# Optimization experiments

Measured on AMD Instinct MI355X. Metric: run time of the kernel, lower is better.

The kernel has to match this reference:

```python
import jax, jax.numpy as jnp
import numpy as np

E = 2048
H = 16
D = E // H  # head_dim = 128
S_SLOTS = 8
EPS = 1e-5


def _linear_params(key, fan_in, fan_out):
    kw, kb = jax.random.split(key)
    lim = 1.0 / np.sqrt(fan_in)
    W = jax.random.uniform(kw, (fan_out, fan_in), jnp.float32, -lim, lim)
    b = jax.random.uniform(kb, (fan_out,), jnp.float32, -lim, lim)
    return W, b


def setup_inputs() -> dict:
    key = jax.random.key(0)
    ks = jax.random.split(key, 10)
    x = jax.random.normal(ks[0], (2, 2048, E), jnp.float32)
    thought_slots = jax.random.normal(ks[1], (S_SLOTS, E), jnp.float32)
    Wq, bq = _linear_params(ks[2], E, E)
    Wk, bk = _linear_params(ks[3], E, E)
    Wv, bv = _linear_params(ks[4], E, E)
    Wtq, btq = _linear_params(ks[5], E, E)
    Wtk, btk = _linear_params(ks[6], E, E)
    Wtv, btv = _linear_params(ks[7], E, E)
    Wo, bo = _linear_params(ks[8], E, E)
    gamma = jnp.ones((E,), jnp.float32)
    beta = jnp.zeros((E,), jnp.float32)
    return dict(x=x, thought_slots=thought_slots, Wq=Wq, bq=bq, Wk=Wk, bk=bk,
                Wv=Wv, bv=bv, Wtq=Wtq, btq=btq, Wtk=Wtk, btk=btk,
                Wtv=Wtv, btv=btv, Wo=Wo, bo=bo, gamma=gamma, beta=beta)


def _heads(t, B):
    # [B, S, E] -> [B, H, S, D]
    return t.reshape(B, -1, H, D).transpose(0, 2, 1, 3)


def reference(x, thought_slots, Wq, bq, Wk, bk, Wv, bv,
              Wtq, btq, Wtk, btk, Wtv, btv, Wo, bo, gamma, beta):
    B, S, _ = x.shape
    scale = 1.0 / np.sqrt(D)

    # regular self-attention stream
    q = _heads(x @ Wq.T + bq, B)
    k = _heads(x @ Wk.T + bk, B)
    v = _heads(x @ Wv.T + bv, B)
    attn = jax.nn.softmax(jnp.einsum('bhqd,bhkd->bhqk', q, k) * scale, axis=-1)
    regular_out = jnp.einsum('bhqk,bhkd->bhqd', attn, v)

    # thought cross-attention stream (keys/values from learned slots)
    slots = jnp.broadcast_to(thought_slots, (B, S_SLOTS, thought_slots.shape[-1]))
    t_q = _heads(x @ Wtq.T + btq, B)
    t_k = _heads(slots @ Wtk.T + btk, B)
    t_v = _heads(slots @ Wtv.T + btv, B)
    t_attn = jax.nn.softmax(jnp.einsum('bhqd,bhkd->bhqk', t_q, t_k) * scale, axis=-1)
    thought_out = jnp.einsum('bhqk,bhkd->bhqd', t_attn, t_v)

    # merge heads, combine, layernorm, output projection
    combined = (regular_out + thought_out).transpose(0, 2, 1, 3).reshape(B, S, E)
    mu = jnp.mean(combined, axis=-1, keepdims=True)
    var = jnp.var(combined, axis=-1, keepdims=True)
    normed = (combined - mu) * jax.lax.rsqrt(var + EPS) * gamma + beta
    return normed @ Wo.T + bo
```

## Files before the change

### kernel.cpp

```cpp
#include <hip/hip_runtime.h>
#include <hip/hip_bf16.h>
#include <stdint.h>

typedef __bf16 bf16;
typedef __bf16 bf16x8 __attribute__((ext_vector_type(8)));
typedef __bf16 bf16x4 __attribute__((ext_vector_type(4)));
typedef float f32x4 __attribute__((ext_vector_type(4)));
typedef float f32x16 __attribute__((ext_vector_type(16)));
typedef uint32_t u32x2 __attribute__((ext_vector_type(2)));
typedef uint32_t u32x4 __attribute__((ext_vector_type(4)));

#define E_DIM 2048
#define HEADS 16
#define HD 128
#define SEQ 2048
#define BATCH 2
#define NTOK 4096
#define NSLOT 8

#define QSCALE (0.08838834764831845f * 1.4426950408889634f)

#define WAITV(N) asm volatile("s_waitcnt vmcnt(" #N ")" ::: "memory")

__device__ __forceinline__ void gload_lds16(const void* g, void* lds) {
  __builtin_amdgcn_global_load_lds(
      (const __attribute__((address_space(1))) uint32_t*)g,
      (__attribute__((address_space(3))) uint32_t*)lds, 16, 0, 0);
}

__global__ __launch_bounds__(256) void cvt_f32_bf16_kernel(
    const float* __restrict__ src, bf16* __restrict__ dst, int n8)
{
  for (int i = blockIdx.x * 256 + threadIdx.x; i < n8; i += gridDim.x * 256) {
    const f32x4 a = *(const f32x4*)(src + i * 8);
    const f32x4 b = *(const f32x4*)(src + i * 8 + 4);
    bf16x8 o;
#pragma unroll
    for (int j = 0; j < 4; j++) { o[j] = (bf16)a[j]; o[4 + j] = (bf16)b[j]; }
    *(bf16x8*)(dst + i * 8) = o;
  }
}

struct ProjArgs {
  const bf16* W[4];
  const float* bias[4];
  void* out[4];
  int mode[4];
  float scale[4];
};

__global__ __launch_bounds__(512, 2) void gemm256_kernel(
    const bf16* __restrict__ A, ProjArgs pa, int nbm, int nbn)
{
  __shared__ char As_[2 * 32768];
  __shared__ char Bs_[2 * 32768];

  const int nwg = gridDim.x;
  const int qch = nwg >> 3;
  const int wg = (blockIdx.x & 7) * qch + (blockIdx.x >> 3);
  const int bm = wg % nbm;
  const int rest = wg / nbm;
  const int bn = rest % nbn;
  const int z = rest / nbn;

  const bf16* __restrict__ W = pa.W[z];
  const float* __restrict__ bias = pa.bias[z];
  void* __restrict__ out = pa.out[z];
  const int mode = pa.mode[z];
  const float scale = pa.scale[z];

  const int tid = threadIdx.x;
  const int lane = tid & 63;
  const int w = tid >> 6;
  const int wr = w >> 2;
  const int wc = w & 3;
  const int g = lane >> 4, c = lane & 15;

  const int srow = tid >> 3;
  const int sslot = tid & 7;
  const int scol = (sslot ^ (srow & 7)) * 8;
  const bf16* Abase = A + (size_t)(bm * 256) * 2048;
  const bf16* Bbase = W + (size_t)(bn * 256) * 2048;

  auto stageU = [&](const bf16* gbase, char* lds, int T, int u) {
    char* dst = lds + (T & 1) * 32768 + u * 16384;
    const int k0 = T * 64;
#pragma unroll
    for (int j = 0; j < 2; j++) {
      const int r = u * 128 + srow + j * 64;
      gload_lds16(gbase + (size_t)r * 2048 + k0 + scol,
                  dst + (size_t)(srow + j * 64) * 128 + sslot * 16);
    }
  };

  f32x4 acc[8][4] = {};
  bf16x8 bfr[4][2];

  stageU(Bbase, Bs_, 0, 0); stageU(Bbase, Bs_, 0, 1);
  stageU(Abase, As_, 0, 0); stageU(Abase, As_, 0, 1);
  stageU(Bbase, Bs_, 1, 0); stageU(Bbase, Bs_, 1, 1);
  stageU(Abase, As_, 1, 0);
  WAITV(6);
  __builtin_amdgcn_s_barrier();

  const int NT = 2048 / 64;
  for (int t = 0; t < NT; t++) {
    const int d = t & 1;
    const char* Aq = As_ + d * 32768;
    const char* Bq = Bs_ + d * 32768;
#pragma unroll
    for (int q = 0; q < 4; q++) {
      bf16x8 af[2][2];
      if (q == 0) {
#pragma unroll
        for (int n = 0; n < 4; n++)
#pragma unroll
          for (int kk = 0; kk < 2; kk++) {
            const int row = wc * 64 + n * 16 + c;
            bfr[n][kk] = *(const bf16x8*)(Bq + (size_t)row * 128 +
                                          (((kk * 4 + g) ^ (c & 7)) * 16));
          }
      }
#pragma unroll
      for (int mi2 = 0; mi2 < 2; mi2++)
#pragma unroll
        for (int kk = 0; kk < 2; kk++) {
          const int row = wr * 128 + (q * 2 + mi2) * 16 + c;
          af[mi2][kk] = *(const bf16x8*)(Aq + (size_t)row * 128 +
                                         (((kk * 4 + g) ^ (c & 7)) * 16));
        }

      __builtin_amdgcn_s_barrier();

      if (q == 0)      { if (t + 1 < NT) stageU(Abase, As_, t + 1, 1); }
      else if (q == 1) { if (t + 2 < NT) stageU(Bbase, Bs_, t + 2, 0); }
      else if (q == 2) { if (t + 2 < NT) stageU(Bbase, Bs_, t + 2, 1); }
      else             { if (t + 2 < NT) stageU(Abase, As_, t + 2, 0); }

      __builtin_amdgcn_s_setprio(1);
#pragma unroll
      for (int mi2 = 0; mi2 < 2; mi2++)
#pragma unroll
        for (int n = 0; n < 4; n++)
#pragma unroll
          for (int kk = 0; kk < 2; kk++)
            acc[q * 2 + mi2][n] = __builtin_amdgcn_mfma_f32_16x16x32_bf16(
                af[mi2][kk], bfr[n][kk], acc[q * 2 + mi2][n], 0, 0, 0);
      __builtin_amdgcn_s_setprio(0);

      if (q == 3) {
        if (t < NT - 2)       { WAITV(6); }
        else if (t == NT - 2) { WAITV(0); }
      }
      __builtin_amdgcn_s_barrier();
    }
  }

#pragma unroll
  for (int mi = 0; mi < 8; mi++) {
#pragma unroll
    for (int n = 0; n < 4; n++) {
      const int col = bn * 256 + wc * 64 + n * 16 + c;
      const float bv = bias[col];
#pragma unroll
      for (int j = 0; j < 4; j++) {
        const int row = bm * 256 + wr * 128 + mi * 16 + g * 4 + j;
        const float v = (acc[mi][n][j] + bv) * scale;
        if (mode == 0) {
          ((float*)out)[(size_t)row * E_DIM + col] = v;
        } else {
          const int b = row >> 11, s = row & 2047;
          const int h = col >> 7, d2 = col & 127;
          size_t idx;
          if (mode == 1) idx = (((size_t)(b * HEADS + h)) * SEQ + s) * HD + d2;
          else           idx = (((size_t)(b * HEADS + h)) * HD + d2) * SEQ + s;
          ((bf16*)out)[idx] = (bf16)v;
        }
      }
    }
  }
}

__global__ __launch_bounds__(256) void gemm_nt_kernel(
    const bf16* __restrict__ A, ProjArgs pa, int M, int N, int K)
{
  __shared__ bf16 As[2][128 * 32];
  __shared__ bf16 Bs[2][128 * 32];

  const int z = blockIdx.z;
  const bf16* __restrict__ W = pa.W[z];
  const float* __restrict__ bias = pa.bias[z];
  void* __restrict__ out = pa.out[z];
  const int mode = pa.mode[z];
  const float scale = pa.scale[z];

  const int tid = threadIdx.x;
  const int lane = tid & 63;
  const int w = tid >> 6;
  const int wr = w >> 1, wc = w & 1;
  const int g = lane >> 4, c = lane & 15;
  const int bm = blockIdx.x, bn = blockIdx.y;

  f32x4 acc[4][4] = {};

  const int srow = lane >> 2;
  const int scol = (lane & 3) * 8;
  const bf16* Ab = A + (size_t)(bm * 128 + srow) * K + scol;
  const bf16* Wb = W + (size_t)(bn * 128 + srow) * K + scol;

  auto stage = [&](int k0, int buf) {
#pragma unroll
    for (int i = 0; i < 2; ++i) {
      const int chunk = w * 2 + i;
      gload_lds16(Ab + (size_t)(chunk * 16) * K + k0, (char*)(&As[buf][0]) + chunk * 1024);
      gload_lds16(Wb + (size_t)(chunk * 16) * K + k0, (char*)(&Bs[buf][0]) + chunk * 1024);
    }
  };

  stage(0, 0);
  __syncthreads();
  int cur = 0;

  for (int k0 = 0; k0 < K; k0 += 32) {
    if (k0 + 32 < K) stage(k0 + 32, cur ^ 1);
    bf16x8 af[4], bfr[4];
#pragma unroll
    for (int m = 0; m < 4; m++)
      af[m] = *(const bf16x8*)(&As[cur][0] + (wr * 64 + m * 16 + c) * 32 + g * 8);
#pragma unroll
    for (int n = 0; n < 4; n++)
      bfr[n] = *(const bf16x8*)(&Bs[cur][0] + (wc * 64 + n * 16 + c) * 32 + g * 8);
#pragma unroll
    for (int m = 0; m < 4; m++)
#pragma unroll
      for (int n = 0; n < 4; n++)
        acc[m][n] = __builtin_amdgcn_mfma_f32_16x16x32_bf16(af[m], bfr[n], acc[m][n], 0, 0, 0);
    __syncthreads();
    cur ^= 1;
  }

#pragma unroll
  for (int m = 0; m < 4; m++) {
#pragma unroll
    for (int n = 0; n < 4; n++) {
      const int col = bn * 128 + wc * 64 + n * 16 + c;
      const float bv = bias[col];
#pragma unroll
      for (int j = 0; j < 4; j++) {
        const int row = bm * 128 + wr * 64 + m * 16 + g * 4 + j;
        const float v = (acc[m][n][j] + bv) * scale;
        if (mode == 0) {
          ((float*)out)[(size_t)row * N + col] = v;
        } else {
          const int b = row >> 11, s = row & 2047;
          const int h = col >> 7, d = col & 127;
          size_t idx;
          if (mode == 1) idx = (((size_t)(b * HEADS + h)) * SEQ + s) * HD + d;
          else           idx = (((size_t)(b * HEADS + h)) * HD + d) * SEQ + s;
          ((bf16*)out)[idx] = (bf16)v;
        }
      }
    }
  }
}

__global__ __launch_bounds__(256) void slots_proj_kernel(
    const float* __restrict__ slots,
    const float* __restrict__ Wk, const float* __restrict__ bk,
    const float* __restrict__ Wv, const float* __restrict__ bv,
    float* __restrict__ tk, float* __restrict__ tv)
{
  const int col = blockIdx.x * 256 + threadIdx.x;
  const int slot = blockIdx.y;
  const int mat = blockIdx.z;
  const float* W = mat ? Wv : Wk;
  const float* bias = mat ? bv : bk;
  float* out = mat ? tv : tk;
  const float* xr = slots + (size_t)slot * E_DIM;
  const float* wr = W + (size_t)col * E_DIM;
  float acc = 0.f;
  for (int k = 0; k < E_DIM; k += 4) {
    const f32x4 a = *(const f32x4*)(xr + k);
    const f32x4 b4 = *(const f32x4*)(wr + k);
#pragma unroll
    for (int i = 0; i < 4; i++) acc += a[i] * b4[i];
  }
  out[(size_t)slot * E_DIM + col] = acc + bias[col];
}

__global__ __launch_bounds__(512) void flash_attn_kernel(
    const bf16* __restrict__ Qg, const bf16* __restrict__ Kg,
    const bf16* __restrict__ Vtg, bf16* __restrict__ Og)
{
  __shared__ char Ks[2][64 * 256];
  __shared__ char Vs[2][128 * 128];

  const int orig = blockIdx.x;
  const int logical = (orig & 7) * 32 + (orig >> 3);
  const int qt = logical & 7;
  const int bh = logical >> 3;

  const int tid = threadIdx.x;
  const int lane = tid & 63;
  const int w = tid >> 6;
  const int q = lane & 31;
  const int hi = lane >> 5;
  const int b = bh >> 4, h = bh & 15;
  const int q0 = qt * 256 + w * 32;

  const bf16* Qb = Qg + ((size_t)bh * SEQ + q0) * HD;
  const bf16* Kb = Kg + (size_t)bh * SEQ * HD;
  const bf16* Vb = Vtg + (size_t)bh * HD * SEQ;

  auto stage = [&](int kv0, int buf) {
#pragma unroll
    for (int i = 0; i < 2; i++) {
      const int p = (tid + i * 512) * 16;
      { const int r = p >> 8; const int s16 = (p >> 4) & 15;
        gload_lds16(Kb + (size_t)(kv0 + r) * HD + (s16 ^ (r & 15)) * 8, &Ks[buf][0] + p); }
      { const int r = p >> 7; const int s8 = (p >> 4) & 7;
        gload_lds16(Vb + (size_t)r * SEQ + kv0 + (s8 ^ (r & 7)) * 8, &Vs[buf][0] + p); }
    }
  };

  bf16x8 qf[8];
#pragma unroll
  for (int kc = 0; kc < 8; kc++)
    qf[kc] = *(const bf16x8*)(Qb + (size_t)q * HD + kc * 16 + hi * 8);

  stage(0, 0);
  __syncthreads();
  int cur = 0;

  f32x16 o[4] = {};
  float mrun = -1e30f, lsum = 0.f;

  for (int kv0 = 0; kv0 < SEQ; kv0 += 64) {
    if (kv0 + 64 < SEQ) stage(kv0 + 64, cur ^ 1);

    f32x16 st[2] = {};
    __builtin_amdgcn_s_setprio(1);
#pragma unroll
    for (int kc = 0; kc < 8; kc++) {
#pragma unroll
      for (int blk = 0; blk < 2; blk++) {
        const int rt = blk * 32 + q;
        const int sl = (2 * kc + hi) ^ (rt & 15);
        const bf16x8 kf = *(const bf16x8*)(&Ks[cur][0] + rt * 256 + sl * 16);
        st[blk] = __builtin_amdgcn_mfma_f32_32x32x16_bf16(kf, qf[kc], st[blk], 0, 0, 0);
      }
    }
    __builtin_amdgcn_s_setprio(0);

    float t[16];
#pragma unroll
    for (int i = 0; i < 16; i++) t[i] = fmaxf(st[0][i], st[1][i]);
#pragma unroll
    for (int s2 = 8; s2 > 0; s2 >>= 1)
#pragma unroll
      for (int i = 0; i < 8; i++) if (i < s2) t[i] = fmaxf(t[i], t[i + s2]);
    float lm = t[0];
    lm = fmaxf(lm, __shfl_xor(lm, 32));

    float fsc = 1.0f;
    if (__any(lm > mrun + 8.0f)) {
      const float mn = fmaxf(mrun, lm);
      fsc = exp2f(mrun - mn);
      mrun = mn;
#pragma unroll
      for (int db = 0; db < 4; db++)
#pragma unroll
        for (int i = 0; i < 16; i++) o[db][i] *= fsc;
    }

    float ps0 = 0.f, ps1 = 0.f, ps2 = 0.f, ps3 = 0.f;
#pragma unroll
    for (int blk = 0; blk < 2; blk++)
#pragma unroll
      for (int i = 0; i < 16; i += 4) {
        const float p0 = exp2f(st[blk][i]     - mrun);
        const float p1 = exp2f(st[blk][i + 1] - mrun);
        const float p2 = exp2f(st[blk][i + 2] - mrun);
        const float p3 = exp2f(st[blk][i + 3] - mrun);
        st[blk][i] = p0; st[blk][i + 1] = p1; st[blk][i + 2] = p2; st[blk][i + 3] = p3;
        ps0 += p0; ps1 += p1; ps2 += p2; ps3 += p3;
      }
    lsum = lsum * fsc + ((ps0 + ps1) + (ps2 + ps3));

    bf16x8 pb[2][2];
#pragma unroll
    for (int blk = 0; blk < 2; blk++)
#pragma unroll
      for (int c2 = 0; c2 < 2; c2++) {
        bf16x4 Lv, Hv;
#pragma unroll
        for (int i = 0; i < 4; i++) {
          Lv[i] = (bf16)st[blk][8 * c2 + i];
          Hv[i] = (bf16)st[blk][8 * c2 + 4 + i];
        }
        const u32x2 Lu = __builtin_bit_cast(u32x2, Lv);
        const u32x2 Hu = __builtin_bit_cast(u32x2, Hv);
        const uint32_t s0 = hi ? Lu.x : Hu.x;
        const uint32_t s1 = hi ? Lu.y : Hu.y;
        const uint32_t x0 = (uint32_t)__shfl_xor((int)s0, 32);
        const uint32_t x1 = (uint32_t)__shfl_xor((int)s1, 32);
        u32x4 bv;
        bv.x = hi ? x0 : Lu.x;
        bv.y = hi ? x1 : Lu.y;
        bv.z = hi ? Hu.x : x0;
        bv.w = hi ? Hu.y : x1;
        pb[blk][c2] = __builtin_bit_cast(bf16x8, bv);
      }

    __builtin_amdgcn_s_setprio(1);
#pragma unroll
    for (int db = 0; db < 4; db++) {
      const int rt = db * 32 + q;
#pragma unroll
      for (int blk = 0; blk < 2; blk++)
#pragma unroll
        for (int c2 = 0; c2 < 2; c2++) {
          const int sl = (blk * 4 + c2 * 2 + hi) ^ (rt & 7);
          const bf16x8 vf = *(const bf16x8*)(&Vs[cur][0] + rt * 128 + sl * 16);
          o[db] = __builtin_amdgcn_mfma_f32_32x32x16_bf16(vf, pb[blk][c2], o[db], 0, 0, 0);
        }
    }
    __builtin_amdgcn_s_setprio(0);

    __syncthreads();
    cur ^= 1;
  }

  const float lt = lsum + __shfl_xor(lsum, 32);
  const float linv = 1.0f / lt;
  bf16* Orow = Og + ((size_t)b * SEQ + q0 + q) * E_DIM + h * HD;
#pragma unroll
  for (int db = 0; db < 4; db++)
#pragma unroll
    for (int g4 = 0; g4 < 4; g4++) {
      bf16x4 ov;
#pragma unroll
      for (int i = 0; i < 4; i++) ov[i] = (bf16)(o[db][g4 * 4 + i] * linv);
      *(bf16x4*)(Orow + db * 32 + g4 * 8 + hi * 4) = ov;
    }
}

__global__ __launch_bounds__(256) void thought_ln_kernel(
    const bf16* __restrict__ TQ, const float* __restrict__ TK,
    const float* __restrict__ TV, const bf16* __restrict__ ATT,
    const float* __restrict__ gamma, const float* __restrict__ beta,
    bf16* __restrict__ Y)
{
  __shared__ float wsum[4], wsq[4];
  const int tid = threadIdx.x;
  const int lane = tid & 63;
  const int w = tid >> 6;
  const int tok = blockIdx.x;
  const int b = tok >> 11, s = tok & 2047;
  const int e0 = tid * 8;
  const int h = e0 >> 7;
  const int d0 = e0 & 127;

  const bf16x8 av = *(const bf16x8*)(ATT + (size_t)tok * E_DIM + e0);
  float v[8];
#pragma unroll
  for (int i = 0; i < 8; i++) v[i] = (float)av[i];

  const bf16x8 qv8 = *(const bf16x8*)(TQ + (((size_t)(b * HEADS + h)) * SEQ + s) * HD + d0);
  float qv[8];
#pragma unroll
  for (int i = 0; i < 8; i++) qv[i] = (float)qv8[i];

  float dts[NSLOT];
#pragma unroll
  for (int sl = 0; sl < NSLOT; sl++) {
    const float* tkr = TK + (size_t)sl * E_DIM + e0;
    const f32x4 k0 = *(const f32x4*)(tkr);
    const f32x4 k1 = *(const f32x4*)(tkr + 4);
    float dp = 0.f;
#pragma unroll
    for (int i = 0; i < 4; i++) dp += qv[i] * k0[i] + qv[4 + i] * k1[i];
    dp += __shfl_xor(dp, 1);
    dp += __shfl_xor(dp, 2);
    dp += __shfl_xor(dp, 4);
    dp += __shfl_xor(dp, 8);
    dts[sl] = dp;
  }
  float mx = dts[0];
#pragma unroll
  for (int sl = 1; sl < NSLOT; sl++) mx = fmaxf(mx, dts[sl]);
  float p[NSLOT], den = 0.f;
#pragma unroll
  for (int sl = 0; sl < NSLOT; sl++) { p[sl] = exp2f(dts[sl] - mx); den += p[sl]; }
  const float dinv = 1.0f / den;
#pragma unroll
  for (int sl = 0; sl < NSLOT; sl++) {
    const float pn = p[sl] * dinv;
    const float* tvr = TV + (size_t)sl * E_DIM + e0;
    const f32x4 v0 = *(const f32x4*)(tvr);
    const f32x4 v1 = *(const f32x4*)(tvr + 4);
#pragma unroll
    for (int i = 0; i < 4; i++) { v[i] += pn * v0[i]; v[4 + i] += pn * v1[i]; }
  }

  float sm = 0.f, sq = 0.f;
#pragma unroll
  for (int i = 0; i < 8; i++) { sm += v[i]; sq += v[i] * v[i]; }
#pragma unroll
  for (int d = 1; d < 64; d <<= 1) { sm += __shfl_xor(sm, d); sq += __shfl_xor(sq, d); }
  if (lane == 0) { wsum[w] = sm; wsq[w] = sq; }
  __syncthreads();
  const float ts = wsum[0] + wsum[1] + wsum[2] + wsum[3];
  const float tq2 = wsq[0] + wsq[1] + wsq[2] + wsq[3];
  const float mean = ts * (1.f / E_DIM);
  const float var = tq2 * (1.f / E_DIM) - mean * mean;
  const float rstd = rsqrtf(var + 1e-5f);
  const f32x4 g0 = *(const f32x4*)(gamma + e0);
  const f32x4 g1 = *(const f32x4*)(gamma + e0 + 4);
  const f32x4 b0 = *(const f32x4*)(beta + e0);
  const f32x4 b1 = *(const f32x4*)(beta + e0 + 4);
  bf16x8 outv;
#pragma unroll
  for (int i = 0; i < 4; i++) {
    outv[i]     = (bf16)((v[i]     - mean) * rstd * g0[i] + b0[i]);
    outv[4 + i] = (bf16)((v[4 + i] - mean) * rstd * g1[i] + b1[i]);
  }
  *(bf16x8*)(Y + (size_t)tok * E_DIM + e0) = outv;
}

extern "C" void kernel_launch(void* const* d_in, const int* in_sizes, int n_in,
                              void* d_out, int out_size, void* d_ws, size_t ws_size,
                              hipStream_t stream) {
  (void)in_sizes; (void)n_in; (void)out_size; (void)ws_size;
  const float* x     = (const float*)d_in[0];
  const float* slots = (const float*)d_in[1];
  const float* Wq  = (const float*)d_in[2];   const float* bq  = (const float*)d_in[3];
  const float* Wk  = (const float*)d_in[4];   const float* bk  = (const float*)d_in[5];
  const float* Wv  = (const float*)d_in[6];   const float* bv  = (const float*)d_in[7];
  const float* Wtq = (const float*)d_in[8];   const float* btq = (const float*)d_in[9];
  const float* Wtk = (const float*)d_in[10];  const float* btk = (const float*)d_in[11];
  const float* Wtv = (const float*)d_in[12];  const float* btv = (const float*)d_in[13];
  const float* Wo  = (const float*)d_in[14];  const float* bo  = (const float*)d_in[15];
  const float* gamma = (const float*)d_in[16];
  const float* beta  = (const float*)d_in[17];

  uint8_t* ws = (uint8_t*)d_ws;
  const size_t BUF  = (size_t)NTOK * E_DIM * sizeof(bf16);
  const size_t WBUF = (size_t)E_DIM * E_DIM * sizeof(bf16);
  bf16* xb   = (bf16*)(ws + 0 * BUF);
  bf16* qb   = (bf16*)(ws + 1 * BUF);
  bf16* kb   = (bf16*)(ws + 2 * BUF);
  bf16* vtb  = (bf16*)(ws + 3 * BUF);
  bf16* tqb  = (bf16*)(ws + 4 * BUF);
  bf16* attb = (bf16*)(ws + 5 * BUF);
  bf16* nrmb = qb;
  uint8_t* wp = ws + 6 * BUF;
  bf16* Wqb  = (bf16*)(wp + 0 * WBUF);
  bf16* Wkb  = (bf16*)(wp + 1 * WBUF);
  bf16* Wvb  = (bf16*)(wp + 2 * WBUF);
  bf16* Wtqb = (bf16*)(wp + 3 * WBUF);
  bf16* Wob  = (bf16*)(wp + 4 * WBUF);
  float* tkb = (float*)(wp + 5 * WBUF);
  float* tvb = (float*)(wp + 5 * WBUF + 128 * 1024);

  const int WN8 = E_DIM * E_DIM / 8;
  const int XN8 = NTOK * E_DIM / 8;
  cvt_f32_bf16_kernel<<<dim3(2048), 256, 0, stream>>>(x, xb, XN8);
  cvt_f32_bf16_kernel<<<dim3(1024), 256, 0, stream>>>(Wq, Wqb, WN8);
  cvt_f32_bf16_kernel<<<dim3(1024), 256, 0, stream>>>(Wk, Wkb, WN8);
  cvt_f32_bf16_kernel<<<dim3(1024), 256, 0, stream>>>(Wv, Wvb, WN8);
  cvt_f32_bf16_kernel<<<dim3(1024), 256, 0, stream>>>(Wtq, Wtqb, WN8);
  cvt_f32_bf16_kernel<<<dim3(1024), 256, 0, stream>>>(Wo, Wob, WN8);

  ProjArgs pa;
  pa.W[0] = Wqb;  pa.bias[0] = bq;  pa.out[0] = qb;  pa.mode[0] = 1; pa.scale[0] = QSCALE;
  pa.W[1] = Wkb;  pa.bias[1] = bk;  pa.out[1] = kb;  pa.mode[1] = 1; pa.scale[1] = 1.0f;
  pa.W[2] = Wvb;  pa.bias[2] = bv;  pa.out[2] = vtb; pa.mode[2] = 2; pa.scale[2] = 1.0f;
  pa.W[3] = Wtqb; pa.bias[3] = btq; pa.out[3] = tqb; pa.mode[3] = 1; pa.scale[3] = QSCALE;
  gemm256_kernel<<<dim3(16 * 8 * 4), 512, 0, stream>>>(xb, pa, 16, 8);

  slots_proj_kernel<<<dim3(E_DIM / 256, NSLOT, 2), 256, 0, stream>>>(
      slots, Wtk, btk, Wtv, btv, tkb, tvb);

  flash_attn_kernel<<<dim3((SEQ / 256) * BATCH * HEADS), 512, 0, stream>>>(
      qb, kb, vtb, attb);
  thought_ln_kernel<<<dim3(NTOK), 256, 0, stream>>>(
      tqb, tkb, tvb, attb, gamma, beta, nrmb);

  ProjArgs po;
  po.W[0] = Wob; po.bias[0] = bo; po.out[0] = d_out; po.mode[0] = 0; po.scale[0] = 1.0f;
  po.W[1] = po.W[2] = po.W[3] = Wob;
  po.bias[1] = po.bias[2] = po.bias[3] = bo;
  po.out[1] = po.out[2] = po.out[3] = d_out;
  po.mode[1] = po.mode[2] = po.mode[3] = 0;
  po.scale[1] = po.scale[2] = po.scale[3] = 1.0f;
  gemm_nt_kernel<<<dim3(NTOK / 128, E_DIM / 128, 1), 256, 0, stream>>>(
      nrmb, po, NTOK, E_DIM, E_DIM);
}
```

Baseline: 466.1 us.

## Software-pipeline flash attention PV with triple buffering; batch weight conversions

The flash attention loop now delays the P·V MFMA of each tile by one iteration, using a triple-buffered K/V LDS ring so the previous tile's PV product overlaps the current tile's QK and softmax. The rescale of the output accumulator moves after the delayed PV. Separately, the five weight f32→bf16 conversion launches are merged into one 2D-grid kernel to cut launch overhead. LDS use grows by half, which may reduce occupancy, and the setprio hints around PV were dropped.

```diff
diff --git a/kernel.cpp b/kernel.cpp
--- a/kernel.cpp
+++ b/kernel.cpp
@@ -37,6 +37,22 @@
     bf16x8 o;
 #pragma unroll
     for (int j = 0; j < 4; j++) { o[j] = (bf16)a[j]; o[4 + j] = (bf16)b[j]; }
+    *(bf16x8*)(dst + i * 8) = o;
+  }
+}
+
+struct CvtArgs { const float* src[5]; bf16* dst[5]; };
+
+__global__ __launch_bounds__(256) void cvt5_kernel(CvtArgs a, int n8)
+{
+  const float* __restrict__ src = a.src[blockIdx.y];
+  bf16* __restrict__ dst = a.dst[blockIdx.y];
+  for (int i = blockIdx.x * 256 + threadIdx.x; i < n8; i += gridDim.x * 256) {
+    const f32x4 x = *(const f32x4*)(src + i * 8);
+    const f32x4 y = *(const f32x4*)(src + i * 8 + 4);
+    bf16x8 o;
+#pragma unroll
+    for (int j = 0; j < 4; j++) { o[j] = (bf16)x[j]; o[4 + j] = (bf16)y[j]; }
     *(bf16x8*)(dst + i * 8) = o;
   }
 }
@@ -292,8 +308,8 @@
     const bf16* __restrict__ Qg, const bf16* __restrict__ Kg,
     const bf16* __restrict__ Vtg, bf16* __restrict__ Og)
 {
-  __shared__ char Ks[2][64 * 256];
-  __shared__ char Vs[2][128 * 128];
+  __shared__ char Ks[3][64 * 256];
+  __shared__ char Vs[3][128 * 128];
 
   const int orig = blockIdx.x;
   const int logical = (orig & 7) * 32 + (orig >> 3);
@@ -317,9 +333,9 @@
     for (int i = 0; i < 2; i++) {
       const int p = (tid + i * 512) * 16;
       { const int r = p >> 8; const int s16 = (p >> 4) & 15;
-        gload_lds16(Kb + (size_t)(kv0 + r) * HD + (s16 ^ (r & 15)) * 8, &Ks[buf][0] + p); }
+        gload_lds16(Kb + (size_t)(kv0 + r) * HD + (s16 ^ (r & 15)) * 8, &Ks[0][0] + buf * 16384 + p); }
       { const int r = p >> 7; const int s8 = (p >> 4) & 7;
-        gload_lds16(Vb + (size_t)r * SEQ + kv0 + (s8 ^ (r & 7)) * 8, &Vs[buf][0] + p); }
+        gload_lds16(Vb + (size_t)r * SEQ + kv0 + (s8 ^ (r & 7)) * 8, &Vs[0][0] + buf * 16384 + p); }
     }
   };
 
@@ -328,17 +344,21 @@
   for (int kc = 0; kc < 8; kc++)
     qf[kc] = *(const bf16x8*)(Qb + (size_t)q * HD + kc * 16 + hi * 8);
 
+  f32x16 o[4] = {};
+  float mrun = -1e30f, lsum = 0.f;
+  bf16x8 pbo[2][2];
+
   stage(0, 0);
   __syncthreads();
-  int cur = 0;
-
-  f32x16 o[4] = {};
-  float mrun = -1e30f, lsum = 0.f;
-
-  for (int kv0 = 0; kv0 < SEQ; kv0 += 64) {
-    if (kv0 + 64 < SEQ) stage(kv0 + 64, cur ^ 1);
+
+  int prv = 2, cur = 0, nxt = 1;
+  const int NT = SEQ / 64;
+
+  for (int t = 0; t < NT; t++) {
+    if (t + 1 < NT) stage((t + 1) * 64, nxt);
 
     f32x16 st[2] = {};
+    const char* Kc = &Ks[0][0] + cur * 16384;
     __builtin_amdgcn_s_setprio(1);
 #pragma unroll
     for (int kc = 0; kc < 8; kc++) {
@@ -346,31 +366,27 @@
       for (int blk = 0; blk < 2; blk++) {
         const int rt = blk * 32 + q;
         const int sl = (2 * kc + hi) ^ (rt & 15);
-        const bf16x8 kf = *(const bf16x8*)(&Ks[cur][0] + rt * 256 + sl * 16);
+        const bf16x8 kf = *(const bf16x8*)(Kc + rt * 256 + sl * 16);
         st[blk] = __builtin_amdgcn_mfma_f32_32x32x16_bf16(kf, qf[kc], st[blk], 0, 0, 0);
       }
     }
     __builtin_amdgcn_s_setprio(0);
 
-    float t[16];
-#pragma unroll
-    for (int i = 0; i < 16; i++) t[i] = fmaxf(st[0][i], st[1][i]);
+    float tm[16];
+#pragma unroll
+    for (int i = 0; i < 16; i++) tm[i] = fmaxf(st[0][i], st[1][i]);
 #pragma unroll
     for (int s2 = 8; s2 > 0; s2 >>= 1)
 #pragma unroll
-      for (int i = 0; i < 8; i++) if (i < s2) t[i] = fmaxf(t[i], t[i + s2]);
-    float lm = t[0];
+      for (int i = 0; i < 8; i++) if (i < s2) tm[i] = fmaxf(tm[i], tm[i + s2]);
+    float lm = tm[0];
     lm = fmaxf(lm, __shfl_xor(lm, 32));
-
     float fsc = 1.0f;
-    if (__any(lm > mrun + 8.0f)) {
+    const bool resc = __any(lm > mrun + 8.0f);
+    if (resc) {
       const float mn = fmaxf(mrun, lm);
       fsc = exp2f(mrun - mn);
       mrun = mn;
-#pragma unroll
-      for (int db = 0; db < 4; db++)
-#pragma unroll
-        for (int i = 0; i < 16; i++) o[db][i] *= fsc;
     }
 
     float ps0 = 0.f, ps1 = 0.f, ps2 = 0.f, ps3 = 0.f;
@@ -387,7 +403,7 @@
       }
     lsum = lsum * fsc + ((ps0 + ps1) + (ps2 + ps3));
 
-    bf16x8 pb[2][2];
+    bf16x8 pbn[2][2];
 #pragma unroll
     for (int blk = 0; blk < 2; blk++)
 #pragma unroll
@@ -409,10 +425,43 @@
         bv.y = hi ? x1 : Lu.y;
         bv.z = hi ? Hu.x : x0;
         bv.w = hi ? Hu.y : x1;
-        pb[blk][c2] = __builtin_bit_cast(bf16x8, bv);
-      }
-
-    __builtin_amdgcn_s_setprio(1);
+        pbn[blk][c2] = __builtin_bit_cast(bf16x8, bv);
+      }
+
+    if (t > 0) {
+      const char* Vc = &Vs[0][0] + prv * 16384;
+#pragma unroll
+      for (int db = 0; db < 4; db++) {
+        const int rt = db * 32 + q;
+#pragma unroll
+        for (int blk = 0; blk < 2; blk++)
+#pragma unroll
+          for (int c2 = 0; c2 < 2; c2++) {
+            const int sl = (blk * 4 + c2 * 2 + hi) ^ (rt & 7);
+            const bf16x8 vf = *(const bf16x8*)(Vc + rt * 128 + sl * 16);
+            o[db] = __builtin_amdgcn_mfma_f32_32x32x16_bf16(vf, pbn ? pbo[blk][c2] : pbo[blk][c2], o[db], 0, 0, 0);
+          }
+      }
+    }
+
+    if (resc) {
+#pragma unroll
+      for (int db = 0; db < 4; db++)
+#pragma unroll
+        for (int i = 0; i < 16; i++) o[db][i] *= fsc;
+    }
+
+#pragma unroll
+    for (int blk = 0; blk < 2; blk++)
+#pragma unroll
+      for (int c2 = 0; c2 < 2; c2++) pbo[blk][c2] = pbn[blk][c2];
+
+    __syncthreads();
+    const int tmp = prv; prv = cur; cur = nxt; nxt = tmp;
+  }
+
+  {
+    const char* Vc = &Vs[0][0] + prv * 16384;
 #pragma unroll
     for (int db = 0; db < 4; db++) {
       const int rt = db * 32 + q;
@@ -421,14 +470,10 @@
 #pragma unroll
         for (int c2 = 0; c2 < 2; c2++) {
           const int sl = (blk * 4 + c2 * 2 + hi) ^ (rt & 7);
-          const bf16x8 vf = *(const bf16x8*)(&Vs[cur][0] + rt * 128 + sl * 16);
-          o[db] = __builtin_amdgcn_mfma_f32_32x32x16_bf16(vf, pb[blk][c2], o[db], 0, 0, 0);
+          const bf16x8 vf = *(const bf16x8*)(Vc + rt * 128 + sl * 16);
+          o[db] = __builtin_amdgcn_mfma_f32_32x32x16_bf16(vf, pbo[blk][c2], o[db], 0, 0, 0);
         }
     }
-    __builtin_amdgcn_s_setprio(0);
-
-    __syncthreads();
-    cur ^= 1;
   }
 
   const float lt = lsum + __shfl_xor(lsum, 32);
@@ -566,11 +611,13 @@
   const int WN8 = E_DIM * E_DIM / 8;
   const int XN8 = NTOK * E_DIM / 8;
   cvt_f32_bf16_kernel<<<dim3(2048), 256, 0, stream>>>(x, xb, XN8);
-  cvt_f32_bf16_kernel<<<dim3(1024), 256, 0, stream>>>(Wq, Wqb, WN8);
-  cvt_f32_bf16_kernel<<<dim3(1024), 256, 0, stream>>>(Wk, Wkb, WN8);
-  cvt_f32_bf16_kernel<<<dim3(1024), 256, 0, stream>>>(Wv, Wvb, WN8);
-  cvt_f32_bf16_kernel<<<dim3(1024), 256, 0, stream>>>(Wtq, Wtqb, WN8);
-  cvt_f32_bf16_kernel<<<dim3(1024), 256, 0, stream>>>(Wo, Wob, WN8);
+  CvtArgs ca;
+  ca.src[0] = Wq;  ca.dst[0] = Wqb;
+  ca.src[1] = Wk;  ca.dst[1] = Wkb;
+  ca.src[2] = Wv;  ca.dst[2] = Wvb;
+  ca.src[3] = Wtq; ca.dst[3] = Wtqb;
+  ca.src[4] = Wo;  ca.dst[4] = Wob;
+  cvt5_kernel<<<dim3(1024, 5), 256, 0, stream>>>(ca, WN8);
 
   ProjArgs pa;
   pa.W[0] = Wqb;  pa.bias[0] = bq;  pa.out[0] = qb;  pa.mode[0] = 1; pa.scale[0] = QSCALE;
```

After: 448.7 us. 1.04x faster.
